# Optimization experiments

Hardware: AMD Instinct MI355X
Metric: run time of the kernel (lower is better)

Reference implementation:

```python
import jax, jax.numpy as jnp
import numpy as np

HEAD_DIM = 64
EPS = 1e-06


def yat_dense(x, kernel, bias):
    # YatDense (nmn): y = (x.W)^2 / (||x - w||^2 + eps) * alpha_scale + b
    dot = x @ kernel                                  # [..., F]
    x_sq = jnp.sum(x * x, axis=-1, keepdims=True)     # [..., 1]
    w_sq = jnp.sum(kernel * kernel, axis=0)           # [F]
    dist = x_sq + w_sq - 2.0 * dot                    # squared euclidean distance
    y = (dot * dot) / (dist + EPS)
    feats = kernel.shape[1]
    scale = np.sqrt(feats) / np.log1p(feats)          # alpha=1 scaling
    return y * jnp.asarray(scale, x.dtype) + bias


def apply_rope(q, k):
    # q,k: [B,H,T,D]; interleaved-pair rotation, base 10000 (dim=HEAD_DIM)
    B, H, T, D = q.shape
    half = D // 2
    pos = jnp.arange(T, dtype=jnp.float32)
    freqs = 10000.0 ** (-jnp.arange(half, dtype=jnp.float32) / half)
    ang = pos[:, None] * freqs[None, :]               # [T, half]
    sin = jnp.sin(ang)[None, None, :, :, None]        # [1,1,T,half,1]
    cos = jnp.cos(ang)[None, None, :, :, None]

    def rot(t):
        ts = t.reshape(B, H, T, half, 2)
        t0, t1 = ts[..., 0:1], ts[..., 1:2]
        out = jnp.concatenate([t0 * cos - t1 * sin, t1 * cos + t0 * sin], axis=-1)
        return out.reshape(B, H, T, D)

    return rot(q), rot(k)


def setup_inputs() -> dict:
    key = jax.random.key(0)
    B, T, C, H = 2, 2048, 1024, 16
    k1, k2, k3, k4, k5 = jax.random.split(key, 5)
    x = jax.random.normal(k1, (B, T, C), dtype=jnp.float32)
    # causal mask, broadcast over batch
    mask = jnp.broadcast_to(jnp.tril(jnp.ones((T, T), dtype=bool))[None], (B, T, T))
    s = 1.0 / np.sqrt(C)
    w_attn = jax.random.normal(k2, (C, 3 * C), dtype=jnp.float32) * s
    b_attn = jnp.zeros((3 * C,), dtype=jnp.float32)
    w_proj = jax.random.normal(k3, (C, C), dtype=jnp.float32) * s
    b_proj = jnp.zeros((C,), dtype=jnp.float32)
    return {"x": x, "mask": mask, "w_attn": w_attn, "b_attn": b_attn,
            "w_proj": w_proj, "b_proj": b_proj}


def reference(x, mask, w_attn, b_attn, w_proj, b_proj):
    B, T, C = x.shape
    H = C // HEAD_DIM
    qkv = yat_dense(x, w_attn, b_attn)                     # [B,T,3C]
    qkv = qkv.reshape(B, T, 3, H, HEAD_DIM)
    q, k, v = jnp.moveaxis(qkv, 2, 0)                      # each [B,T,H,hd]
    q = jnp.swapaxes(q, 1, 2)                              # [B,H,T,hd]
    k = jnp.swapaxes(k, 1, 2)
    v = jnp.swapaxes(v, 1, 2)
    q, k = apply_rope(q, k)
    scale = jnp.asarray(np.sqrt(HEAD_DIM), x.dtype)
    attn = jnp.einsum('bhqd,bhkd->bhqk', q, k) / scale     # [B,H,T,T]
    neg = jnp.finfo(x.dtype).min
    attn = jnp.where(mask[:, None, :, :], attn, neg)
    attn = jax.nn.softmax(attn, axis=-1)
    out = jnp.einsum('bhqk,bhkd->bhqd', attn, v)           # [B,H,T,hd]
    out = jnp.swapaxes(out, 1, 2).reshape(B, T, C)
    return yat_dense(out, w_proj, b_proj)
```

## Files before the change

kernel.cpp:

```cpp
#include <hip/hip_runtime.h>
#include <hip/hip_bf16.h>
#include <cmath>

#define BB 2
#define TT 2048
#define CC 1024
#define HH 16
#define DD 64
#define ROWS (BB*TT)
#define N1 (3*CC)
#define EPS 1e-6f

using short8 = __attribute__((ext_vector_type(8))) short;
using f32x4  = __attribute__((ext_vector_type(4))) float;

__device__ __forceinline__ void gl_lds16(const __hip_bfloat16* g, unsigned short* l) {
    __builtin_amdgcn_global_load_lds(
        (const __attribute__((address_space(1))) unsigned int*)(g),
        (__attribute__((address_space(3))) unsigned int*)(l), 16, 0, 0);
}

__device__ __forceinline__ unsigned int bf16pair(float a, float b) {
    __hip_bfloat16 ha = (__hip_bfloat16)a, hb = (__hip_bfloat16)b;
    unsigned short ua = *(unsigned short*)&ha, ub = *(unsigned short*)&hb;
    return (unsigned int)ua | ((unsigned int)ub << 16);
}

__device__ __forceinline__ float bf2f(unsigned short u) {
    unsigned int v = (unsigned int)u << 16;
    return *(float*)&v;
}

__global__ void aux_rowsq(const float* __restrict__ X, float* __restrict__ xsq,
                          __hip_bfloat16* __restrict__ Xb, float* __restrict__ osq,
                          float* __restrict__ rope,
                          float* __restrict__ wsqa, float* __restrict__ wsqp) {
    int blk = blockIdx.x;
    int t = threadIdx.x;
    if (blk >= ROWS) {
        int idx = (blk - ROWS) * 256 + t;
        if (idx < N1) wsqa[idx] = 0.f;
        if (idx < CC) wsqp[idx] = 0.f;
        if (idx < TT * 32) {
            int tt = idx >> 5, i = idx & 31;
            double freq = pow(10000.0, -(double)i / 32.0);
            float ang = (float)tt * (float)freq;
            rope[idx * 2 + 0] = cosf(ang);
            rope[idx * 2 + 1] = sinf(ang);
        }
        return;
    }
    int row = blk;
    const float* xr = X + (size_t)row * CC;
    __hip_bfloat16* br = Xb + (size_t)row * CC;
    float p = 0.f;
#pragma unroll
    for (int i = 0; i < 4; ++i) {
        float v = xr[t + i * 256];
        p += v * v;
        br[t + i * 256] = (__hip_bfloat16)v;
    }
#pragma unroll
    for (int off = 32; off > 0; off >>= 1) p += __shfl_xor(p, off, 64);
    __shared__ float s4[4];
    if ((t & 63) == 0) s4[t >> 6] = p;
    __syncthreads();
    if (t == 0) { xsq[row] = s4[0] + s4[1] + s4[2] + s4[3]; osq[row] = 0.f; }
}

__global__ void transpose2(const float* __restrict__ Wa, __hip_bfloat16* __restrict__ WaT,
                           float* __restrict__ wsqa,
                           const float* __restrict__ Wp, __hip_bfloat16* __restrict__ WpT,
                           float* __restrict__ wsqp) {
    const float* W; __hip_bfloat16* Wt; float* wsq; int N;
    if (blockIdx.z == 0) { W = Wa; Wt = WaT; wsq = wsqa; N = N1; }
    else { if (blockIdx.x >= 16) return; W = Wp; Wt = WpT; wsq = wsqp; N = CC; }
    const int K = CC;
    __shared__ unsigned short tile[64][65];
    int n0 = blockIdx.x * 64, k0 = blockIdx.y * 64;
    int c = threadIdx.x & 63, rg = threadIdx.x >> 6;
    float part = 0.f;
#pragma unroll
    for (int rr = 0; rr < 16; ++rr) {
        int r = rg + rr * 4;
        float f = W[(size_t)(k0 + r) * N + n0 + c];
        __hip_bfloat16 h = (__hip_bfloat16)f;
        tile[r][c] = *(unsigned short*)&h;
        part += f * f;
    }
    atomicAdd(&wsq[n0 + c], part);
    __syncthreads();
#pragma unroll
    for (int rr = 0; rr < 16; ++rr) {
        int r = rg + rr * 4;
        unsigned short u = tile[c][r];
        Wt[(size_t)(n0 + r) * K + k0 + c] = *(__hip_bfloat16*)&u;
    }
}

__global__ __launch_bounds__(256) void yat_gemm_qkv2(
    const __hip_bfloat16* __restrict__ A,
    const __hip_bfloat16* __restrict__ Bt,
    const float* __restrict__ xsq, const float* __restrict__ wsq,
    const float* __restrict__ bias,
    __hip_bfloat16* __restrict__ Qb, __hip_bfloat16* __restrict__ Kb,
    __hip_bfloat16* __restrict__ Vb, float scale) {
    const int K = CC;
    __shared__ __align__(16) unsigned short As0[128 * 32], As1[128 * 32];
    __shared__ __align__(16) unsigned short Bs0[128 * 32], Bs1[128 * 32];
    int tid = threadIdx.x;
    int wave = tid >> 6, lane = tid & 63, quad = lane >> 4, l16 = lane & 15;
    int wr = wave >> 1, wc = wave & 1;
    int m0 = blockIdx.y * 128, n0 = blockIdx.x * 128;

    f32x4 acc[4][4];
#pragma unroll
    for (int mt = 0; mt < 4; ++mt)
#pragma unroll
        for (int nt = 0; nt < 4; ++nt) acc[mt][nt] = f32x4{0.f, 0.f, 0.f, 0.f};

    int srow = lane >> 2, soff = (lane & 3) << 3;
    for (int k0 = 0; k0 < K; k0 += 64) {
        __syncthreads();
#pragma unroll
        for (int i = 0; i < 2; ++i) {
            int rowc = (wave * 2 + i) * 16;
            const __hip_bfloat16* ap = A + (size_t)(m0 + rowc + srow) * K + k0 + soff;
            gl_lds16(ap,      As0 + rowc * 32);
            gl_lds16(ap + 32, As1 + rowc * 32);
            const __hip_bfloat16* bp = Bt + (size_t)(n0 + rowc + srow) * K + k0 + soff;
            gl_lds16(bp,      Bs0 + rowc * 32);
            gl_lds16(bp + 32, Bs1 + rowc * 32);
        }
        __syncthreads();
#pragma unroll
        for (int h = 0; h < 2; ++h) {
            const unsigned short* Ah = h ? As1 : As0;
            const unsigned short* Bh = h ? Bs1 : Bs0;
            short8 af[4], bf[4];
#pragma unroll
            for (int mt = 0; mt < 4; ++mt)
                af[mt] = *(const short8*)(Ah + (wr * 64 + mt * 16 + l16) * 32 + quad * 8);
#pragma unroll
            for (int nt = 0; nt < 4; ++nt)
                bf[nt] = *(const short8*)(Bh + (wc * 64 + nt * 16 + l16) * 32 + quad * 8);
#pragma unroll
            for (int mt = 0; mt < 4; ++mt)
#pragma unroll
                for (int nt = 0; nt < 4; ++nt)
                    acc[mt][nt] = __builtin_amdgcn_mfma_f32_16x16x32_bf16(af[mt], bf[nt], acc[mt][nt], 0, 0, 0);
        }
    }
    int mb = m0 + wr * 64 + quad * 4;
#pragma unroll
    for (int nt = 0; nt < 4; ++nt) {
        int col = n0 + wc * 64 + nt * 16 + l16;
        float wq = wsq[col], bs = bias[col];
        int sec = col >> 10, cc2 = col & 1023;
        int h = cc2 >> 6, d = cc2 & 63;
        __hip_bfloat16* dst = (sec == 0) ? Qb : ((sec == 1) ? Kb : Vb);
#pragma unroll
        for (int mt = 0; mt < 4; ++mt) {
#pragma unroll
            for (int r = 0; r < 4; ++r) {
                int row = mb + mt * 16 + r;
                float dot = acc[mt][nt][r];
                float dist = xsq[row] + wq - 2.f * dot + EPS;
                float y = dot * dot / dist * scale + bs;
                int t = row & (TT - 1), bI = row >> 11;
                dst[(((size_t)bI * HH + h) * TT + t) * DD + d] = (__hip_bfloat16)y;
            }
        }
    }
}

__global__ __launch_bounds__(256) void ropek_vtrans(
    unsigned short* __restrict__ Kb, const unsigned short* __restrict__ Vb,
    __hip_bfloat16* __restrict__ Vtb, const float* __restrict__ rope) {
    int bh = blockIdx.y, t0 = blockIdx.x * 64, tid = threadIdx.x;
    __shared__ unsigned short vt[64][72];
    int r = tid >> 2, g = tid & 3;
    const unsigned short* src = Vb + ((size_t)bh * TT + t0 + r) * DD + g * 16;
    *(uint4*)&vt[r][g * 16]     = *(const uint4*)src;
    *(uint4*)&vt[r][g * 16 + 8] = *(const uint4*)(src + 8);
    {
        int t = t0 + r;
        unsigned short* kp = Kb + ((size_t)bh * TT + t) * DD + g * 16;
        union U8 { uint4 v; unsigned short s[8]; } k0v, k1v, o0, o1;
        k0v.v = *(const uint4*)kp;
        k1v.v = *(const uint4*)(kp + 8);
        const float* rp = rope + (size_t)t * 64 + g * 16;
#pragma unroll
        for (int u = 0; u < 8; ++u) {
            float c = rp[2 * u], sn = rp[2 * u + 1];
            unsigned short ev = (u < 4) ? k0v.s[2 * u]     : k1v.s[2 * u - 8];
            unsigned short ov = (u < 4) ? k0v.s[2 * u + 1] : k1v.s[2 * u - 7];
            float f0 = bf2f(ev), f1 = bf2f(ov);
            unsigned int pr = bf16pair(f0 * c - f1 * sn, f1 * c + f0 * sn);
            if (u < 4) ((unsigned int*)&o0)[u] = pr;
            else       ((unsigned int*)&o1)[u - 4] = pr;
        }
        *(uint4*)kp = o0.v;
        *(uint4*)(kp + 8) = o1.v;
    }
    __syncthreads();
    union U8b { uint4 v; unsigned short s[8]; };
#pragma unroll
    for (int p = 0; p < 2; ++p) {
        int d = (tid >> 3) + p * 32, tl = (tid & 7) * 8;
        U8b w;
#pragma unroll
        for (int j = 0; j < 8; ++j) w.s[j] = vt[tl + j][d];
        *(uint4*)(Vtb + ((size_t)bh * DD + d) * TT + t0 + tl) = w.v;
    }
}

__global__ __launch_bounds__(256, 3) void attn_mfma8(
    const __hip_bfloat16* __restrict__ Qb, const __hip_bfloat16* __restrict__ Kb,
    const __hip_bfloat16* __restrict__ Vtb, const float* __restrict__ rope,
    __hip_bfloat16* __restrict__ out, float* __restrict__ osq) {
    const float QSC = 0.125f * 1.44269504f;
    int i = blockIdx.x;
    int xcd = i & 7, jj = (i >> 3) & 3, s = i >> 5;
    int bh = xcd + 8 * jj;
    int b = bh >> 4, h = bh & 15;
    int tid = threadIdx.x;
    int wave = tid >> 6, lane = tid & 63, quad = lane >> 4, l16 = lane & 15;

    __shared__ __align__(16) unsigned short Ks[2][2][64 * 32];
    __shared__ __align__(16) unsigned short Vs[2][2][64 * 32];
    __shared__ __align__(16) unsigned short Ps[4][16 * 72];
    unsigned short* pp = &Ps[wave][0];

    const __hip_bfloat16* Qbase = Qb + (size_t)bh * TT * DD;
    const __hip_bfloat16* Kbase = Kb + (size_t)bh * TT * DD;
    const __hip_bfloat16* Vbase = Vtb + (size_t)bh * DD * TT;

    int srow = lane >> 2, soff = (lane & 3) * 8;
    short8 ones8;
#pragma unroll
    for (int u = 0; u < 8; ++u) ones8[u] = (short)0x3F80;

    int u0, u1, nunits;
    if (s < 8)       { u0 = s;      u1 = 15 - s; nunits = 2; }
    else if (s < 16) { u0 = s + 8;  u1 = 0;      nunits = 1; }
    else             { u0 = 47 - s; u1 = 0;      nunits = 1; }

    for (int un = 0; un < nunits; ++un) {
        int qblk = un ? u1 : u0;
        int qw = qblk * 64 + wave * 16;
        short8 qf0, qf1;
        {
            int t = qw + l16;
            const unsigned short* qr = (const unsigned short*)(Qbase + (size_t)t * DD) + quad * 8;
            union S8 { short8 v; unsigned short s[8]; } r0, r1, o0v, o1v;
            r0.v = *(const short8*)qr;
            r1.v = *(const short8*)(qr + 32);
            const float* rpa = rope + (size_t)t * 64 + quad * 8;
            const float* rpb = rpa + 32;
#pragma unroll
            for (int u = 0; u < 4; ++u) {
                float c = rpa[2 * u] * QSC, sn = rpa[2 * u + 1] * QSC;
                float e = bf2f(r0.s[2 * u]), o = bf2f(r0.s[2 * u + 1]);
                ((unsigned int*)&o0v)[u] = bf16pair(e * c - o * sn, o * c + e * sn);
                float c2 = rpb[2 * u] * QSC, sn2 = rpb[2 * u + 1] * QSC;
                float e2 = bf2f(r1.s[2 * u]), o2 = bf2f(r1.s[2 * u + 1]);
                ((unsigned int*)&o1v)[u] = bf16pair(e2 * c2 - o2 * sn2, o2 * c2 + e2 * sn2);
            }
            qf0 = o0v.v;
            qf1 = o1v.v;
        }
        f32x4 acc_o[4];
#pragma unroll
        for (int mt = 0; mt < 4; ++mt) acc_o[mt] = f32x4{0.f, 0.f, 0.f, 0.f};
        f32x4 acc_l = {0.f, 0.f, 0.f, 0.f};
        int q_g = qw + l16;

        __syncthreads();
        gl_lds16(Kbase + (size_t)(wave * 16 + srow) * DD + soff,      &Ks[0][0][wave * 512]);
        gl_lds16(Kbase + (size_t)(wave * 16 + srow) * DD + 32 + soff, &Ks[0][1][wave * 512]);
        gl_lds16(Vbase + (size_t)(wave * 16 + srow) * TT + soff,      &Vs[0][0][wave * 512]);
        gl_lds16(Vbase + (size_t)(wave * 16 + srow) * TT + 32 + soff, &Vs[0][1][wave * 512]);

        for (int kt = 0; kt <= qblk; ++kt) {
            int cur = kt & 1;
            int k0 = kt * 64;
            __syncthreads();
            if (kt < qblk) {
                int nb = cur ^ 1, kn = k0 + 64;
                gl_lds16(Kbase + (size_t)(kn + wave * 16 + srow) * DD + soff,      &Ks[nb][0][wave * 512]);
                gl_lds16(Kbase + (size_t)(kn + wave * 16 + srow) * DD + 32 + soff, &Ks[nb][1][wave * 512]);
                gl_lds16(Vbase + (size_t)(wave * 16 + srow) * TT + kn + soff,      &Vs[nb][0][wave * 512]);
                gl_lds16(Vbase + (size_t)(wave * 16 + srow) * TT + kn + 32 + soff, &Vs[nb][1][wave * 512]);
            }
            f32x4 accs[4];
#pragma unroll
            for (int mt = 0; mt < 4; ++mt) {
                short8 kf0 = *(const short8*)(&Ks[cur][0][(mt * 16 + l16) * 32 + quad * 8]);
                short8 kf1 = *(const short8*)(&Ks[cur][1][(mt * 16 + l16) * 32 + quad * 8]);
                f32x4 z = {0.f, 0.f, 0.f, 0.f};
                z = __builtin_amdgcn_mfma_f32_16x16x32_bf16(kf0, qf0, z, 0, 0, 0);
                accs[mt] = __builtin_amdgcn_mfma_f32_16x16x32_bf16(kf1, qf1, z, 0, 0, 0);
            }
            int limit = (kt == qblk) ? q_g : 0x7FFFFFFF;
#pragma unroll
            for (int mt = 0; mt < 4; ++mt) {
                int keyb = k0 + mt * 16 + quad * 4;
                float p0 = exp2f(accs[mt][0]);
                float p1 = exp2f(accs[mt][1]);
                float p2 = exp2f(accs[mt][2]);
                float p3 = exp2f(accs[mt][3]);
                p0 = (keyb + 0 <= limit) ? p0 : 0.f;
                p1 = (keyb + 1 <= limit) ? p1 : 0.f;
                p2 = (keyb + 2 <= limit) ? p2 : 0.f;
                p3 = (keyb + 3 <= limit) ? p3 : 0.f;
                uint2 w2;
                w2.x = bf16pair(p0, p1);
                w2.y = bf16pair(p2, p3);
                *(uint2*)(pp + l16 * 72 + mt * 16 + quad * 4) = w2;
            }
            short8 pf0 = *(const short8*)(pp + l16 * 72 + quad * 8);
            short8 pf1 = *(const short8*)(pp + l16 * 72 + 32 + quad * 8);
#pragma unroll
            for (int mt = 0; mt < 4; ++mt) {
                short8 vf0 = *(const short8*)(&Vs[cur][0][(mt * 16 + l16) * 32 + quad * 8]);
                short8 vf1 = *(const short8*)(&Vs[cur][1][(mt * 16 + l16) * 32 + quad * 8]);
                acc_o[mt] = __builtin_amdgcn_mfma_f32_16x16x32_bf16(vf0, pf0, acc_o[mt], 0, 0, 0);
                acc_o[mt] = __builtin_amdgcn_mfma_f32_16x16x32_bf16(vf1, pf1, acc_o[mt], 0, 0, 0);
            }
            acc_l = __builtin_amdgcn_mfma_f32_16x16x32_bf16(ones8, pf0, acc_l, 0, 0, 0);
            acc_l = __builtin_amdgcn_mfma_f32_16x16x32_bf16(ones8, pf1, acc_l, 0, 0, 0);
        }
        float inv = 1.f / acc_l[0];
        float part = 0.f;
#pragma unroll
        for (int mt = 0; mt < 4; ++mt) {
            float o0 = acc_o[mt][0] * inv;
            float o1 = acc_o[mt][1] * inv;
            float o2 = acc_o[mt][2] * inv;
            float o3 = acc_o[mt][3] * inv;
            part += o0 * o0 + o1 * o1 + o2 * o2 + o3 * o3;
            uint2 w2;
            w2.x = bf16pair(o0, o1);
            w2.y = bf16pair(o2, o3);
            *(uint2*)(pp + l16 * 72 + mt * 16 + quad * 4) = w2;
        }
        part += __shfl_xor(part, 16, 64);
        part += __shfl_xor(part, 32, 64);
        if (quad == 0) atomicAdd(&osq[(size_t)b * TT + qw + l16], part);
        int rw = lane >> 2, cg = lane & 3;
        uint4 o0 = *(const uint4*)(pp + rw * 72 + cg * 16);
        uint4 o1 = *(const uint4*)(pp + rw * 72 + cg * 16 + 8);
        __hip_bfloat16* orow = out + (size_t)(b * TT + qw + rw) * CC + h * DD + cg * 16;
        *(uint4*)(orow) = o0;
        *(uint4*)(orow + 8) = o1;
    }
}

template<int TM, int TN, typename OutT>
__global__ __launch_bounds__(256) void yat_gemm_bk64(
    const __hip_bfloat16* __restrict__ A,
    const __hip_bfloat16* __restrict__ Bt,
    const float* __restrict__ xsq, const float* __restrict__ wsq,
    const float* __restrict__ bias, OutT* __restrict__ C,
    int M, int N, int K, float scale) {
    constexpr int MT = TM / 32;
    constexpr int NT = TN / 32;
    constexpr int IA = TM / 64;
    constexpr int IB = TN / 64;
    __shared__ __align__(16) unsigned short As0[TM * 32];
    __shared__ __align__(16) unsigned short As1[TM * 32];
    __shared__ __align__(16) unsigned short Bs0[TN * 32];
    __shared__ __align__(16) unsigned short Bs1[TN * 32];
    int tid = threadIdx.x;
    int wave = tid >> 6, lane = tid & 63, quad = lane >> 4, l16 = lane & 15;
    int wr = wave >> 1, wc = wave & 1;
    int m0 = blockIdx.y * TM, n0 = blockIdx.x * TN;

    f32x4 acc[MT][NT];
#pragma unroll
    for (int mt = 0; mt < MT; ++mt)
#pragma unroll
        for (int nt = 0; nt < NT; ++nt) acc[mt][nt] = f32x4{0.f, 0.f, 0.f, 0.f};

    int srow = lane >> 2, soff = (lane & 3) << 3;
    for (int k0 = 0; k0 < K; k0 += 64) {
        __syncthreads();
#pragma unroll
        for (int i = 0; i < IA; ++i) {
            int rowc = (wave * IA + i) * 16;
            const __hip_bfloat16* ap = A + (size_t)(m0 + rowc + srow) * K + k0 + soff;
            gl_lds16(ap,      As0 + rowc * 32);
            gl_lds16(ap + 32, As1 + rowc * 32);
        }
#pragma unroll
        for (int i = 0; i < IB; ++i) {
            int rowc = (wave * IB + i) * 16;
            const __hip_bfloat16* bp = Bt + (size_t)(n0 + rowc + srow) * K + k0 + soff;
            gl_lds16(bp,      Bs0 + rowc * 32);
            gl_lds16(bp + 32, Bs1 + rowc * 32);
        }
        __syncthreads();
#pragma unroll
        for (int h = 0; h < 2; ++h) {
            const unsigned short* Ah = h ? As1 : As0;
            const unsigned short* Bh = h ? Bs1 : Bs0;
            short8 af[MT], bf[NT];
#pragma unroll
            for (int mt = 0; mt < MT; ++mt)
                af[mt] = *(const short8*)(Ah + (wr * (TM / 2) + mt * 16 + l16) * 32 + quad * 8);
#pragma unroll
            for (int nt = 0; nt < NT; ++nt)
                bf[nt] = *(const short8*)(Bh + (wc * (TN / 2) + nt * 16 + l16) * 32 + quad * 8);
#pragma unroll
            for (int mt = 0; mt < MT; ++mt)
#pragma unroll
                for (int nt = 0; nt < NT; ++nt)
                    acc[mt][nt] = __builtin_amdgcn_mfma_f32_16x16x32_bf16(af[mt], bf[nt], acc[mt][nt], 0, 0, 0);
        }
    }
    int mb = m0 + wr * (TM / 2) + quad * 4;
#pragma unroll
    for (int nt = 0; nt < NT; ++nt) {
        int col = n0 + wc * (TN / 2) + nt * 16 + l16;
        float wq = wsq[col];
        float bs = bias[col];
#pragma unroll
        for (int mt = 0; mt < MT; ++mt) {
#pragma unroll
            for (int r = 0; r < 4; ++r) {
                int row = mb + mt * 16 + r;
                float dot = acc[mt][nt][r];
                float dist = xsq[row] + wq - 2.f * dot + EPS;
                C[(size_t)row * N + col] = (OutT)(dot * dot / dist * scale + bs);
            }
        }
    }
}

extern "C" void kernel_launch(void* const* d_in, const int* in_sizes, int n_in,
                              void* d_out, int out_size, void* d_ws, size_t ws_size,
                              hipStream_t stream) {
    const float* x      = (const float*)d_in[0];
    const float* w_attn = (const float*)d_in[2];
    const float* b_attn = (const float*)d_in[3];
    const float* w_proj = (const float*)d_in[4];
    const float* b_proj = (const float*)d_in[5];
    float* out = (float*)d_out;

    char* ws = (char*)d_ws;
    __hip_bfloat16* xbf  = (__hip_bfloat16*)(ws + 0);
    __hip_bfloat16* aout = (__hip_bfloat16*)(ws + 8388608);
    __hip_bfloat16* watT = (__hip_bfloat16*)(ws + 16777216);
    __hip_bfloat16* wpT  = (__hip_bfloat16*)(ws + 23068672);
    float*          rope = (float*)(ws + 25165824);
    float*          xsq  = (float*)(ws + 25690112);
    float*          osq  = (float*)(ws + 25706496);
    float*          wsqa = (float*)(ws + 25722880);
    float*          wsqp = (float*)(ws + 25735168);
    __hip_bfloat16* Qb   = (__hip_bfloat16*)(ws + 25739264);
    __hip_bfloat16* Kb   = (__hip_bfloat16*)(ws + 34127872);
    __hip_bfloat16* Vb   = (__hip_bfloat16*)(ws + 42516480);
    __hip_bfloat16* Vtb  = (__hip_bfloat16*)(ws + 50905088);

    float scale1 = (float)(sqrt(3072.0) / log1p(3072.0));
    float scale2 = (float)(sqrt(1024.0) / log1p(1024.0));

    aux_rowsq<<<ROWS + 256, 256, 0, stream>>>(x, xsq, xbf, osq, rope, wsqa, wsqp);
    transpose2<<<dim3(48, 16, 2), 256, 0, stream>>>(w_attn, watT, wsqa, w_proj, wpT, wsqp);
    yat_gemm_qkv2<<<dim3(N1 / 128, ROWS / 128), 256, 0, stream>>>(
        xbf, watT, xsq, wsqa, b_attn, Qb, Kb, Vb, scale1);
    ropek_vtrans<<<dim3(TT / 64, BB * HH), 256, 0, stream>>>(
        (unsigned short*)Kb, (const unsigned short*)Vb, Vtb, rope);
    attn_mfma8<<<768, 256, 0, stream>>>(Qb, Kb, Vtb, rope, aout, osq);
    yat_gemm_bk64<64, 64, float><<<dim3(CC / 64, ROWS / 64), 256, 0, stream>>>(
        aout, wpT, osq, wsqp, b_proj, out, ROWS, CC, CC, scale2);
}
```

Baseline: 220.6 us.

## Use one query block per attention workgroup with XOR-swizzled P buffer

The attention kernel now launches 1024 workgroups, each handling exactly one 64-row query block with an interleaved ordering of block indices. Previously 768 workgroups had some processing two causal units. The P/O staging buffer in LDS drops its padded stride of 72 for a stride of 64 with an XOR swizzle, which shrinks LDS use and is meant to avoid bank conflicts. Launch bounds go from 3 to 4 workgroups per SM to raise occupancy. The cost is a less even causal workload per block and more register pressure under the tighter bound.

```diff
diff --git a/kernel.cpp b/kernel.cpp
--- a/kernel.cpp
+++ b/kernel.cpp
@@ -215,146 +215,145 @@
     }
 }
 
-__global__ __launch_bounds__(256, 3) void attn_mfma8(
+__global__ __launch_bounds__(256, 4) void attn_mfma10(
     const __hip_bfloat16* __restrict__ Qb, const __hip_bfloat16* __restrict__ Kb,
     const __hip_bfloat16* __restrict__ Vtb, const float* __restrict__ rope,
     __hip_bfloat16* __restrict__ out, float* __restrict__ osq) {
     const float QSC = 0.125f * 1.44269504f;
     int i = blockIdx.x;
-    int xcd = i & 7, jj = (i >> 3) & 3, s = i >> 5;
-    int bh = xcd + 8 * jj;
+    int xcd = i & 7;
+    int r0 = i >> 3;
+    int bh = xcd + 8 * (r0 & 3);
+    int rr = r0 >> 2;
+    int v = rr & 7, s2 = rr >> 3;
+    int qblk = (s2 == 0) ? v : (s2 == 1) ? (15 - v) : (s2 == 2) ? (16 + v) : (31 - v);
     int b = bh >> 4, h = bh & 15;
     int tid = threadIdx.x;
     int wave = tid >> 6, lane = tid & 63, quad = lane >> 4, l16 = lane & 15;
 
     __shared__ __align__(16) unsigned short Ks[2][2][64 * 32];
     __shared__ __align__(16) unsigned short Vs[2][2][64 * 32];
-    __shared__ __align__(16) unsigned short Ps[4][16 * 72];
+    __shared__ __align__(16) unsigned short Ps[4][16 * 64];
     unsigned short* pp = &Ps[wave][0];
+    int sw = l16 & 7;
 
     const __hip_bfloat16* Qbase = Qb + (size_t)bh * TT * DD;
     const __hip_bfloat16* Kbase = Kb + (size_t)bh * TT * DD;
     const __hip_bfloat16* Vbase = Vtb + (size_t)bh * DD * TT;
 
+    int qw = qblk * 64 + wave * 16;
+    short8 qf0, qf1;
+    {
+        int t = qw + l16;
+        const unsigned short* qr = (const unsigned short*)(Qbase + (size_t)t * DD) + quad * 8;
+        union S8 { short8 v; unsigned short s[8]; } r0v, r1v, o0v, o1v;
+        r0v.v = *(const short8*)qr;
+        r1v.v = *(const short8*)(qr + 32);
+        const float* rpa = rope + (size_t)t * 64 + quad * 8;
+        const float* rpb = rpa + 32;
+#pragma unroll
+        for (int u = 0; u < 4; ++u) {
+            float c = rpa[2 * u] * QSC, sn = rpa[2 * u + 1] * QSC;
+            float e = bf2f(r0v.s[2 * u]), o = bf2f(r0v.s[2 * u + 1]);
+            ((unsigned int*)&o0v)[u] = bf16pair(e * c - o * sn, o * c + e * sn);
+            float c2 = rpb[2 * u] * QSC, sn2 = rpb[2 * u + 1] * QSC;
+            float e2 = bf2f(r1v.s[2 * u]), o2 = bf2f(r1v.s[2 * u + 1]);
+            ((unsigned int*)&o1v)[u] = bf16pair(e2 * c2 - o2 * sn2, o2 * c2 + e2 * sn2);
+        }
+        qf0 = o0v.v;
+        qf1 = o1v.v;
+    }
+    short8 ones8;
+#pragma unroll
+    for (int u = 0; u < 8; ++u) ones8[u] = (short)0x3F80;
+
+    f32x4 acc_o[4];
+#pragma unroll
+    for (int mt = 0; mt < 4; ++mt) acc_o[mt] = f32x4{0.f, 0.f, 0.f, 0.f};
+    f32x4 acc_l = {0.f, 0.f, 0.f, 0.f};
+
     int srow = lane >> 2, soff = (lane & 3) * 8;
-    short8 ones8;
-#pragma unroll
-    for (int u = 0; u < 8; ++u) ones8[u] = (short)0x3F80;
-
-    int u0, u1, nunits;
-    if (s < 8)       { u0 = s;      u1 = 15 - s; nunits = 2; }
-    else if (s < 16) { u0 = s + 8;  u1 = 0;      nunits = 1; }
-    else             { u0 = 47 - s; u1 = 0;      nunits = 1; }
-
-    for (int un = 0; un < nunits; ++un) {
-        int qblk = un ? u1 : u0;
-        int qw = qblk * 64 + wave * 16;
-        short8 qf0, qf1;
-        {
-            int t = qw + l16;
-            const unsigned short* qr = (const unsigned short*)(Qbase + (size_t)t * DD) + quad * 8;
-            union S8 { short8 v; unsigned short s[8]; } r0, r1, o0v, o1v;
-            r0.v = *(const short8*)qr;
-            r1.v = *(const short8*)(qr + 32);
-            const float* rpa = rope + (size_t)t * 64 + quad * 8;
-            const float* rpb = rpa + 32;
-#pragma unroll
-            for (int u = 0; u < 4; ++u) {
-                float c = rpa[2 * u] * QSC, sn = rpa[2 * u + 1] * QSC;
-                float e = bf2f(r0.s[2 * u]), o = bf2f(r0.s[2 * u + 1]);
-                ((unsigned int*)&o0v)[u] = bf16pair(e * c - o * sn, o * c + e * sn);
-                float c2 = rpb[2 * u] * QSC, sn2 = rpb[2 * u + 1] * QSC;
-                float e2 = bf2f(r1.s[2 * u]), o2 = bf2f(r1.s[2 * u + 1]);
-                ((unsigned int*)&o1v)[u] = bf16pair(e2 * c2 - o2 * sn2, o2 * c2 + e2 * sn2);
-            }
-            qf0 = o0v.v;
-            qf1 = o1v.v;
-        }
-        f32x4 acc_o[4];
-#pragma unroll
-        for (int mt = 0; mt < 4; ++mt) acc_o[mt] = f32x4{0.f, 0.f, 0.f, 0.f};
-        f32x4 acc_l = {0.f, 0.f, 0.f, 0.f};
-        int q_g = qw + l16;
-
+    int q_g = qw + l16;
+
+    gl_lds16(Kbase + (size_t)(wave * 16 + srow) * DD + soff,      &Ks[0][0][wave * 512]);
+    gl_lds16(Kbase + (size_t)(wave * 16 + srow) * DD + 32 + soff, &Ks[0][1][wave * 512]);
+    gl_lds16(Vbase + (size_t)(wave * 16 + srow) * TT + soff,      &Vs[0][0][wave * 512]);
+    gl_lds16(Vbase + (size_t)(wave * 16 + srow) * TT + 32 + soff, &Vs[0][1][wave * 512]);
+
+    for (int kt = 0; kt <= qblk; ++kt) {
+        int cur = kt & 1;
+        int k0 = kt * 64;
         __syncthreads();
-        gl_lds16(Kbase + (size_t)(wave * 16 + srow) * DD + soff,      &Ks[0][0][wave * 512]);
-        gl_lds16(Kbase + (size_t)(wave * 16 + srow) * DD + 32 + soff, &Ks[0][1][wave * 512]);
-        gl_lds16(Vbase + (size_t)(wave * 16 + srow) * TT + soff,      &Vs[0][0][wave * 512]);
-        gl_lds16(Vbase + (size_t)(wave * 16 + srow) * TT + 32 + soff, &Vs[0][1][wave * 512]);
-
-        for (int kt = 0; kt <= qblk; ++kt) {
-            int cur = kt & 1;
-            int k0 = kt * 64;
-            __syncthreads();
-            if (kt < qblk) {
-                int nb = cur ^ 1, kn = k0 + 64;
-                gl_lds16(Kbase + (size_t)(kn + wave * 16 + srow) * DD + soff,      &Ks[nb][0][wave * 512]);
-                gl_lds16(Kbase + (size_t)(kn + wave * 16 + srow) * DD + 32 + soff, &Ks[nb][1][wave * 512]);
-                gl_lds16(Vbase + (size_t)(wave * 16 + srow) * TT + kn + soff,      &Vs[nb][0][wave * 512]);
-                gl_lds16(Vbase + (size_t)(wave * 16 + srow) * TT + kn + 32 + soff, &Vs[nb][1][wave * 512]);
-            }
-            f32x4 accs[4];
-#pragma unroll
-            for (int mt = 0; mt < 4; ++mt) {
-                short8 kf0 = *(const short8*)(&Ks[cur][0][(mt * 16 + l16) * 32 + quad * 8]);
-                short8 kf1 = *(const short8*)(&Ks[cur][1][(mt * 16 + l16) * 32 + quad * 8]);
-                f32x4 z = {0.f, 0.f, 0.f, 0.f};
-                z = __builtin_amdgcn_mfma_f32_16x16x32_bf16(kf0, qf0, z, 0, 0, 0);
-                accs[mt] = __builtin_amdgcn_mfma_f32_16x16x32_bf16(kf1, qf1, z, 0, 0, 0);
-            }
-            int limit = (kt == qblk) ? q_g : 0x7FFFFFFF;
-#pragma unroll
-            for (int mt = 0; mt < 4; ++mt) {
-                int keyb = k0 + mt * 16 + quad * 4;
-                float p0 = exp2f(accs[mt][0]);
-                float p1 = exp2f(accs[mt][1]);
-                float p2 = exp2f(accs[mt][2]);
-                float p3 = exp2f(accs[mt][3]);
-                p0 = (keyb + 0 <= limit) ? p0 : 0.f;
-                p1 = (keyb + 1 <= limit) ? p1 : 0.f;
-                p2 = (keyb + 2 <= limit) ? p2 : 0.f;
-                p3 = (keyb + 3 <= limit) ? p3 : 0.f;
-                uint2 w2;
-                w2.x = bf16pair(p0, p1);
-                w2.y = bf16pair(p2, p3);
-                *(uint2*)(pp + l16 * 72 + mt * 16 + quad * 4) = w2;
-            }
-            short8 pf0 = *(const short8*)(pp + l16 * 72 + quad * 8);
-            short8 pf1 = *(const short8*)(pp + l16 * 72 + 32 + quad * 8);
-#pragma unroll
-            for (int mt = 0; mt < 4; ++mt) {
-                short8 vf0 = *(const short8*)(&Vs[cur][0][(mt * 16 + l16) * 32 + quad * 8]);
-                short8 vf1 = *(const short8*)(&Vs[cur][1][(mt * 16 + l16) * 32 + quad * 8]);
-                acc_o[mt] = __builtin_amdgcn_mfma_f32_16x16x32_bf16(vf0, pf0, acc_o[mt], 0, 0, 0);
-                acc_o[mt] = __builtin_amdgcn_mfma_f32_16x16x32_bf16(vf1, pf1, acc_o[mt], 0, 0, 0);
-            }
-            acc_l = __builtin_amdgcn_mfma_f32_16x16x32_bf16(ones8, pf0, acc_l, 0, 0, 0);
-            acc_l = __builtin_amdgcn_mfma_f32_16x16x32_bf16(ones8, pf1, acc_l, 0, 0, 0);
-        }
-        float inv = 1.f / acc_l[0];
-        float part = 0.f;
+        if (kt < qblk) {
+            int nb = cur ^ 1, kn = k0 + 64;
+            gl_lds16(Kbase + (size_t)(kn + wave * 16 + srow) * DD + soff,      &Ks[nb][0][wave * 512]);
+            gl_lds16(Kbase + (size_t)(kn + wave * 16 + srow) * DD + 32 + soff, &Ks[nb][1][wave * 512]);
+            gl_lds16(Vbase + (size_t)(wave * 16 + srow) * TT + kn + soff,      &Vs[nb][0][wave * 512]);
+            gl_lds16(Vbase + (size_t)(wave * 16 + srow) * TT + kn + 32 + soff, &Vs[nb][1][wave * 512]);
+        }
+        f32x4 accs[4];
 #pragma unroll
         for (int mt = 0; mt < 4; ++mt) {
-            float o0 = acc_o[mt][0] * inv;
-            float o1 = acc_o[mt][1] * inv;
-            float o2 = acc_o[mt][2] * inv;
-            float o3 = acc_o[mt][3] * inv;
-            part += o0 * o0 + o1 * o1 + o2 * o2 + o3 * o3;
+            short8 kf0 = *(const short8*)(&Ks[cur][0][(mt * 16 + l16) * 32 + quad * 8]);
+            short8 kf1 = *(const short8*)(&Ks[cur][1][(mt * 16 + l16) * 32 + quad * 8]);
+            f32x4 z = {0.f, 0.f, 0.f, 0.f};
+            z = __builtin_amdgcn_mfma_f32_16x16x32_bf16(kf0, qf0, z, 0, 0, 0);
+            accs[mt] = __builtin_amdgcn_mfma_f32_16x16x32_bf16(kf1, qf1, z, 0, 0, 0);
+        }
+        int limit = (kt == qblk) ? q_g : 0x7FFFFFFF;
+#pragma unroll
+        for (int mt = 0; mt < 4; ++mt) {
+            int keyb = k0 + mt * 16 + quad * 4;
+            float p0 = exp2f(accs[mt][0]);
+            float p1 = exp2f(accs[mt][1]);
+            float p2 = exp2f(accs[mt][2]);
+            float p3 = exp2f(accs[mt][3]);
+            p0 = (keyb + 0 <= limit) ? p0 : 0.f;
+            p1 = (keyb + 1 <= limit) ? p1 : 0.f;
+            p2 = (keyb + 2 <= limit) ? p2 : 0.f;
+            p3 = (keyb + 3 <= limit) ? p3 : 0.f;
             uint2 w2;
-            w2.x = bf16pair(o0, o1);
-            w2.y = bf16pair(o2, o3);
-            *(uint2*)(pp + l16 * 72 + mt * 16 + quad * 4) = w2;
-        }
-        part += __shfl_xor(part, 16, 64);
-        part += __shfl_xor(part, 32, 64);
-        if (quad == 0) atomicAdd(&osq[(size_t)b * TT + qw + l16], part);
-        int rw = lane >> 2, cg = lane & 3;
-        uint4 o0 = *(const uint4*)(pp + rw * 72 + cg * 16);
-        uint4 o1 = *(const uint4*)(pp + rw * 72 + cg * 16 + 8);
-        __hip_bfloat16* orow = out + (size_t)(b * TT + qw + rw) * CC + h * DD + cg * 16;
-        *(uint4*)(orow) = o0;
-        *(uint4*)(orow + 8) = o1;
-    }
+            w2.x = bf16pair(p0, p1);
+            w2.y = bf16pair(p2, p3);
+            int off = (((mt * 2 + (quad >> 1)) ^ sw) << 3) + ((quad & 1) << 2);
+            *(uint2*)(pp + (l16 << 6) + off) = w2;
+        }
+        short8 pf0 = *(const short8*)(pp + (l16 << 6) + ((quad ^ sw) << 3));
+        short8 pf1 = *(const short8*)(pp + (l16 << 6) + (((4 + quad) ^ sw) << 3));
+#pragma unroll
+        for (int mt = 0; mt < 4; ++mt) {
+            short8 vf0 = *(const short8*)(&Vs[cur][0][(mt * 16 + l16) * 32 + quad * 8]);
+            short8 vf1 = *(const short8*)(&Vs[cur][1][(mt * 16 + l16) * 32 + quad * 8]);
+            acc_o[mt] = __builtin_amdgcn_mfma_f32_16x16x32_bf16(vf0, pf0, acc_o[mt], 0, 0, 0);
+            acc_o[mt] = __builtin_amdgcn_mfma_f32_16x16x32_bf16(vf1, pf1, acc_o[mt], 0, 0, 0);
+        }
+        acc_l = __builtin_amdgcn_mfma_f32_16x16x32_bf16(ones8, pf0, acc_l, 0, 0, 0);
+        acc_l = __builtin_amdgcn_mfma_f32_16x16x32_bf16(ones8, pf1, acc_l, 0, 0, 0);
+    }
+    float inv = 1.f / acc_l[0];
+    float part = 0.f;
+#pragma unroll
+    for (int mt = 0; mt < 4; ++mt) {
+        float o0 = acc_o[mt][0] * inv;
+        float o1 = acc_o[mt][1] * inv;
+        float o2 = acc_o[mt][2] * inv;
+        float o3 = acc_o[mt][3] * inv;
+        part += o0 * o0 + o1 * o1 + o2 * o2 + o3 * o3;
+        uint2 w2;
+        w2.x = bf16pair(o0, o1);
+        w2.y = bf16pair(o2, o3);
+        int off = (((mt * 2 + (quad >> 1)) ^ sw) << 3) + ((quad & 1) << 2);
+        *(uint2*)(pp + (l16 << 6) + off) = w2;
+    }
+    part += __shfl_xor(part, 16, 64);
+    part += __shfl_xor(part, 32, 64);
+    if (quad == 0) atomicAdd(&osq[(size_t)b * TT + qw + l16], part);
+    int rw = lane >> 2, cg = lane & 3, sw2 = rw & 7;
+    uint4 o0 = *(const uint4*)(pp + (rw << 6) + (((cg * 2) ^ sw2) << 3));
+    uint4 o1 = *(const uint4*)(pp + (rw << 6) + (((cg * 2 + 1) ^ sw2) << 3));
+    __hip_bfloat16* orow = out + (size_t)(b * TT + qw + rw) * CC + h * DD + cg * 16;
+    *(uint4*)(orow) = o0;
+    *(uint4*)(orow + 8) = o1;
 }
 
 template<int TM, int TN, typename OutT>
@@ -472,7 +471,7 @@
         xbf, watT, xsq, wsqa, b_attn, Qb, Kb, Vb, scale1);
     ropek_vtrans<<<dim3(TT / 64, BB * HH), 256, 0, stream>>>(
         (unsigned short*)Kb, (const unsigned short*)Vb, Vtb, rope);
-    attn_mfma8<<<768, 256, 0, stream>>>(Qb, Kb, Vtb, rope, aout, osq);
+    attn_mfma10<<<1024, 256, 0, stream>>>(Qb, Kb, Vtb, rope, aout, osq);
     yat_gemm_bk64<64, 64, float><<<dim3(CC / 64, ROWS / 64), 256, 0, stream>>>(
         aout, wpT, osq, wsqp, b_proj, out, ROWS, CC, CC, scale2);
 }
```

New measurement: 222.0 us. About the same (+0.7%).
